# Performance work log

Hardware: AMD Instinct MI355X
Metric: run time of the kernel (lower is better)

The kernel has to match this reference:

```python
import jax, jax.numpy as jnp
import numpy as np

DIM = 1024
HEADS = 16
HEAD_DIM = DIM // HEADS
ROPE_BASE = 500000.0
SCALE = HEAD_DIM ** -0.5


def _rope_cos_sin(T, dtype=jnp.float32):
    inv_freq = 1.0 / (ROPE_BASE ** (jnp.arange(0, HEAD_DIM, 2, dtype=jnp.float32) / HEAD_DIM))
    t = jnp.arange(T, dtype=jnp.float32)
    freqs = t[:, None] * inv_freq[None, :]            # (T, hd/2)
    emb = jnp.concatenate([freqs, freqs], axis=-1)    # (T, hd)
    return jnp.cos(emb).astype(dtype), jnp.sin(emb).astype(dtype)


def _rotate_half(x):
    x1, x2 = jnp.split(x, 2, axis=-1)
    return jnp.concatenate([-x2, x1], axis=-1)


def _apply_rope(x, cos, sin):
    # x: (B,H,T,hd); cos/sin: (T,hd)
    return x * cos + _rotate_half(x) * sin


def setup_inputs() -> dict:
    key = jax.random.key(0)
    k1, k2, k3 = jax.random.split(key, 3)
    B, T = 4, 4096
    x = jax.random.normal(k1, (B, T, DIM), dtype=jnp.float32)
    W_qkv = jax.random.normal(k2, (DIM, 3 * DIM), dtype=jnp.float32) * (DIM ** -0.5)
    W_out = jax.random.normal(k3, (DIM, DIM), dtype=jnp.float32) * (DIM ** -0.5)
    return {"x": x, "W_qkv": W_qkv, "W_out": W_out}


def reference(x, W_qkv, W_out):
    B, T, D = x.shape
    H, hd = HEADS, HEAD_DIM
    qkv = (x @ W_qkv).reshape(B, T, 3, H, hd).transpose(2, 0, 3, 1, 4)  # (3,B,H,T,hd)
    q, k, v = qkv[0], qkv[1], qkv[2]
    cos, sin = _rope_cos_sin(T, q.dtype)
    q = _apply_rope(q, cos, sin)
    k = _apply_rope(k, cos, sin)
    # linear attention: elu+1 feature map
    q_feat = jax.nn.elu(q * SCALE) + 1.0
    k_feat = jax.nn.elu(k) + 1.0
    kv = jnp.einsum('bhtd,bhtv->bhdv', k_feat, v)      # (B,H,hd,hd)
    k_sum = k_feat.sum(axis=2)                          # (B,H,hd)
    denom = jnp.maximum(jnp.einsum('bhtd,bhd->bht', q_feat, k_sum), 1e-6)
    out = jnp.einsum('bhtd,bhdv->bhtv', q_feat, kv) / denom[..., None]
    out = out.transpose(0, 2, 1, 3).reshape(B, T, D)
    return out @ W_out
```

## Files before the change

### kernel.cpp

```cpp
#include <hip/hip_runtime.h>
#include <hip/hip_bf16.h>

typedef __bf16 bf16;
typedef bf16 bf16x4 __attribute__((ext_vector_type(4)));
typedef bf16 bf16x8 __attribute__((ext_vector_type(8)));
typedef float f32x4 __attribute__((ext_vector_type(4)));

#define GLD_LDS16(gptr, lptr) \
  __builtin_amdgcn_global_load_lds((const __attribute__((address_space(1))) unsigned int*)(gptr), \
                                   (__attribute__((address_space(3))) unsigned int*)(lptr), 16, 0, 0)

__global__ __launch_bounds__(256) void f32_to_bf16(const float* __restrict__ in,
                                                   bf16* __restrict__ out) {
  const size_t i = ((size_t)blockIdx.x * 256 + threadIdx.x) * 8;
  float4 a = *(const float4*)(in + i);
  float4 b = *(const float4*)(in + i + 4);
  bf16x8 o;
  o[0] = (bf16)a.x; o[1] = (bf16)a.y; o[2] = (bf16)a.z; o[3] = (bf16)a.w;
  o[4] = (bf16)b.x; o[5] = (bf16)b.y; o[6] = (bf16)b.z; o[7] = (bf16)b.w;
  *(bf16x8*)(out + i) = o;
}

__global__ __launch_bounds__(256) void transpose_f32_bf16(const float* __restrict__ in,
                                                          bf16* __restrict__ out,
                                                          int R, int C) {
  __shared__ float tile[32][33];
  const int bx = blockIdx.x * 32;
  const int by = blockIdx.y * 32;
  const int tx = threadIdx.x & 31;
  const int ty = threadIdx.x >> 5;
#pragma unroll
  for (int i = 0; i < 4; i++) {
    int r = by + ty + i * 8;
    tile[ty + i * 8][tx] = in[(size_t)r * C + bx + tx];
  }
  __syncthreads();
#pragma unroll
  for (int i = 0; i < 4; i++) {
    int r = bx + ty + i * 8;
    out[(size_t)r * R + by + tx] = (bf16)tile[tx][ty + i * 8];
  }
}

__global__ __launch_bounds__(256) void rope_tab(float2* __restrict__ ctab) {
  const int idx = blockIdx.x * 256 + threadIdx.x;
  const int t = idx >> 5, f = idx & 31;
  const float invf = (float)exp(-((double)f / 32.0) * log(500000.0));
  float sn, cs;
  sincosf((float)t * invf, &sn, &cs);
  ctab[idx] = make_float2(cs, sn);
}

__device__ __forceinline__ void gemm256_core(const bf16* __restrict__ A,
                                             const bf16* __restrict__ BT,
                                             const int K, const int m0, const int n0,
                                             bf16* __restrict__ As, bf16* __restrict__ Bs,
                                             f32x4 acc[8][4]) {
  const int tid = threadIdx.x;
  const int lane = tid & 63;
  const int w = tid >> 6;
  const int wm = w >> 2, wn = w & 3;

#pragma unroll
  for (int i = 0; i < 8; i++)
#pragma unroll
    for (int j = 0; j < 4; j++) acc[i][j] = f32x4{0.f, 0.f, 0.f, 0.f};

  const int lch = (tid & 3) ^ ((tid >> 3) & 3);
  const bf16* Ag = A + (size_t)(m0 + (tid >> 2)) * K + lch * 8;
  const bf16* Bg = BT + (size_t)(n0 + (tid >> 2)) * K + lch * 8;
  const int wb = w * 512;

#define STG(kh, db, k0)                                                   \
  do {                                                                    \
    bf16* aD = As + ((db) * 2 + (kh)) * 8192 + wb;                        \
    bf16* bD = Bs + ((db) * 2 + (kh)) * 8192 + wb;                        \
    const size_t go = (size_t)(k0) + (kh) * 32;                           \
    GLD_LDS16(Ag + go, aD);                                               \
    GLD_LDS16(Ag + (size_t)128 * K + go, aD + 4096);                      \
    GLD_LDS16(Bg + go, bD);                                               \
    GLD_LDS16(Bg + (size_t)128 * K + go, bD + 4096);                      \
  } while (0)

  const int fr = lane & 15;
  const int kq = lane >> 4;
  const int frow = fr * 32 + ((kq ^ ((fr >> 1) & 3)) << 3);
  const int aro = wm * 4096;
  const int bro = wn * 2048;

#define LOADFRAGS(kh, db)                                                 \
  const bf16* Ap = As + ((db) * 2 + (kh)) * 8192 + aro + frow;            \
  const bf16* Bp = Bs + ((db) * 2 + (kh)) * 8192 + bro + frow;            \
  bf16x8 af[8], bv[4];                                                    \
  _Pragma("unroll") for (int mi = 0; mi < 8; mi++)                        \
      af[mi] = *(const bf16x8*)(Ap + mi * 512);                           \
  _Pragma("unroll") for (int ni = 0; ni < 4; ni++)                        \
      bv[ni] = *(const bf16x8*)(Bp + ni * 512);

#define MFMA32                                                            \
  __builtin_amdgcn_s_setprio(1);                                          \
  _Pragma("unroll") for (int mi = 0; mi < 8; mi++)                        \
  _Pragma("unroll") for (int ni = 0; ni < 4; ni++)                        \
      acc[mi][ni] = __builtin_amdgcn_mfma_f32_16x16x32_bf16(              \
          af[mi], bv[ni], acc[mi][ni], 0, 0, 0);                          \
  __builtin_amdgcn_s_setprio(0);

  STG(0, 0, 0);
  STG(1, 0, 0);
  if (K > 64) {
    STG(0, 1, 64);
    asm volatile("s_waitcnt vmcnt(8)" ::: "memory");
  } else {
    asm volatile("s_waitcnt vmcnt(4)" ::: "memory");
  }
  __builtin_amdgcn_s_barrier();

  const int NT = K >> 6;
  for (int kt = 0; kt < NT; ++kt) {
    const int db = kt & 1;
    {
      LOADFRAGS(0, db);
      if (kt + 1 < NT) STG(1, db ^ 1, (kt + 1) * 64);
      __builtin_amdgcn_s_barrier();
      asm volatile("s_waitcnt lgkmcnt(0)" ::: "memory");
      __builtin_amdgcn_sched_barrier(0);
      MFMA32;
      if (kt + 1 < NT) asm volatile("s_waitcnt vmcnt(8)" ::: "memory");
      else             asm volatile("s_waitcnt vmcnt(0)" ::: "memory");
      __builtin_amdgcn_s_barrier();
    }
    {
      LOADFRAGS(1, db);
      if (kt + 2 < NT) STG(0, db, (kt + 2) * 64);
      __builtin_amdgcn_s_barrier();
      asm volatile("s_waitcnt lgkmcnt(0)" ::: "memory");
      __builtin_amdgcn_sched_barrier(0);
      MFMA32;
      if (kt + 2 < NT)      asm volatile("s_waitcnt vmcnt(8)" ::: "memory");
      else if (kt + 1 < NT) asm volatile("s_waitcnt vmcnt(4)" ::: "memory");
      __builtin_amdgcn_s_barrier();
    }
  }
#undef STG
#undef LOADFRAGS
#undef MFMA32
}

__device__ __forceinline__ void xcd_tile(int& m0, int& n0) {
  const int gx = gridDim.x;
  const int nwg = gx * gridDim.y;
  const int orig = blockIdx.y * gx + blockIdx.x;
  const int cpx = nwg >> 3;
  const int swb = (orig & 7) * cpx + (orig >> 3);
  m0 = (swb / gx) * 256;
  n0 = (swb % gx) * 256;
}

__global__ __launch_bounds__(512, 2) void gemm_qkv_fused(const bf16* __restrict__ A,
                                                         const bf16* __restrict__ BT,
                                                         const float2* __restrict__ ctab,
                                                         bf16* __restrict__ qfB,
                                                         bf16* __restrict__ kfB,
                                                         bf16* __restrict__ vfB) {
  __shared__ __attribute__((aligned(16))) bf16 As[32768];
  __shared__ __attribute__((aligned(16))) bf16 Bs[32768];
  const int K = 1024;
  int m0, n0;
  xcd_tile(m0, n0);

  f32x4 acc[8][4];
  gemm256_core(A, BT, K, m0, n0, As, Bs, acc);

  const int lane = threadIdx.x & 63;
  const int w = threadIdx.x >> 6;
  const int wm = w >> 2, wn = w & 3;
  const int fr15 = lane & 15;
  const int cb = n0 + wn * 64;
  const int p = cb >> 10;
  const int hh = (cb & 1023) >> 6;
  const int row00 = m0 + wm * 128 + ((lane >> 4) << 2);
  const int b = row00 >> 12;
  const size_t base0 = ((size_t)(b * 16 + hh)) * 4096 * 64;

  if (p == 2) {
#pragma unroll
    for (int mi = 0; mi < 8; mi++)
#pragma unroll
      for (int r = 0; r < 4; r++) {
        const int tloc = (row00 + mi * 16 + r) & 4095;
        bf16* dst = vfB + base0 + (size_t)tloc * 64;
#pragma unroll
        for (int ni = 0; ni < 4; ni++) dst[fr15 + ni * 16] = (bf16)acc[mi][ni][r];
      }
  } else {
    bf16* outp = (p == 0) ? qfB : kfB;
    const float scl = (p == 0) ? 0.125f : 1.0f;
#pragma unroll
    for (int mi = 0; mi < 8; mi++)
#pragma unroll
      for (int r = 0; r < 4; r++) {
        const int tloc = (row00 + mi * 16 + r) & 4095;
        const float2* ct = ctab + tloc * 32;
        bf16* dst = outp + base0 + (size_t)tloc * 64;
#pragma unroll
        for (int ni = 0; ni < 2; ni++) {
          const float2 cs2 = ct[fr15 + ni * 16];
          const float x1 = acc[mi][ni][r], x2 = acc[mi][ni + 2][r];
          const float r1 = (x1 * cs2.x - x2 * cs2.y) * scl;
          const float r2 = (x2 * cs2.x + x1 * cs2.y) * scl;
          dst[fr15 + ni * 16] = (bf16)(r1 > 0.f ? r1 + 1.f : __expf(r1));
          dst[fr15 + ni * 16 + 32] = (bf16)(r2 > 0.f ? r2 + 1.f : __expf(r2));
        }
      }
  }
}

__global__ __launch_bounds__(512, 2) void gemm_bt_f32(const bf16* __restrict__ A,
                                                      const bf16* __restrict__ BT,
                                                      float* __restrict__ C,
                                                      int N, int K) {
  __shared__ __attribute__((aligned(16))) bf16 As[32768];
  __shared__ __attribute__((aligned(16))) bf16 Bs[32768];
  int m0, n0;
  xcd_tile(m0, n0);

  f32x4 acc[8][4];
  gemm256_core(A, BT, K, m0, n0, As, Bs, acc);

  const int lane = threadIdx.x & 63;
  const int w = threadIdx.x >> 6;
  const int wm = w >> 2, wn = w & 3;
  const int col0 = n0 + wn * 64 + (lane & 15);
  const int row00 = m0 + wm * 128 + ((lane >> 4) << 2);
#pragma unroll
  for (int mi = 0; mi < 8; mi++)
#pragma unroll
    for (int ni = 0; ni < 4; ni++)
#pragma unroll
      for (int r = 0; r < 4; r++)
        C[(size_t)(row00 + mi * 16 + r) * N + col0 + ni * 16] = acc[mi][ni][r];
}

__global__ __launch_bounds__(256) void attn_kv(const bf16* __restrict__ kfB,
                                               const bf16* __restrict__ vfB,
                                               float* __restrict__ kvg,
                                               float* __restrict__ ksumg) {
  const int bh = blockIdx.x;
  const int t0 = blockIdx.y * 256;
  __shared__ __attribute__((aligned(16))) float kfs[32][68];
  __shared__ __attribute__((aligned(16))) float vfs[32][68];
  const int tid = threadIdx.x;
  const int dq = tid & 15, g = tid >> 4;
  const int tl = tid >> 3, ch = (tid & 7) * 8;

  f32x4 acc[4];
#pragma unroll
  for (int r = 0; r < 4; r++) acc[r] = f32x4{0.f, 0.f, 0.f, 0.f};
  float ksa[4] = {0.f, 0.f, 0.f, 0.f};

  for (int sc = 0; sc < 8; sc++) {
    const size_t rowb = ((size_t)bh * 4096 + t0 + sc * 32 + tl) * 64 + ch;
    bf16x8 k8 = *(const bf16x8*)(kfB + rowb);
    bf16x8 v8 = *(const bf16x8*)(vfB + rowb);
    f32x4 ka, kb, va, vb;
#pragma unroll
    for (int j = 0; j < 4; j++) {
      ka[j] = (float)k8[j]; kb[j] = (float)k8[j + 4];
      va[j] = (float)v8[j]; vb[j] = (float)v8[j + 4];
    }
    *(f32x4*)&kfs[tl][ch] = ka;
    *(f32x4*)&kfs[tl][ch + 4] = kb;
    *(f32x4*)&vfs[tl][ch] = va;
    *(f32x4*)&vfs[tl][ch + 4] = vb;
    __syncthreads();

#pragma unroll 8
    for (int t = 0; t < 32; t++) {
      f32x4 kq = *(const f32x4*)&kfs[t][dq * 4];
      f32x4 vq = *(const f32x4*)&vfs[t][g * 4];
#pragma unroll
      for (int r = 0; r < 4; r++) {
#pragma unroll
        for (int c = 0; c < 4; c++) acc[r][c] += kq[r] * vq[c];
      }
      if (g == 0) {
#pragma unroll
        for (int r = 0; r < 4; r++) ksa[r] += kq[r];
      }
    }
    __syncthreads();
  }

#pragma unroll
  for (int r = 0; r < 4; r++)
#pragma unroll
    for (int c = 0; c < 4; c++)
      atomicAdd(&kvg[(size_t)bh * 4096 + (dq * 4 + r) * 64 + g * 4 + c], acc[r][c]);
  if (g == 0) {
#pragma unroll
    for (int r = 0; r < 4; r++) atomicAdd(&ksumg[bh * 64 + dq * 4 + r], ksa[r]);
  }
}

__global__ __launch_bounds__(256) void attn_out(const bf16* __restrict__ qfB,
                                                const float* __restrict__ kvg,
                                                const float* __restrict__ ksumg,
                                                bf16* __restrict__ attn) {
  const int bh = blockIdx.y;
  const int b = bh >> 4, h = bh & 15;
  const int t0 = blockIdx.x * 64;
  __shared__ __attribute__((aligned(16))) float qf[64][68];
  __shared__ __attribute__((aligned(16))) float kvs[64][64];
  __shared__ __attribute__((aligned(16))) float ksums[64];
  const int tid = threadIdx.x;

#pragma unroll
  for (int j = 0; j < 2; j++) {
    int chunk = tid + 256 * j;
    int tl = chunk >> 3, col = (chunk & 7) * 8;
    bf16x8 r = *(const bf16x8*)(qfB + ((size_t)bh * 4096 + t0 + tl) * 64 + col);
    f32x4 a, bb;
#pragma unroll
    for (int q = 0; q < 4; q++) { a[q] = (float)r[q]; bb[q] = (float)r[q + 4]; }
    *(f32x4*)&qf[tl][col] = a;
    *(f32x4*)&qf[tl][col + 4] = bb;
  }
#pragma unroll
  for (int j = 0; j < 4; j++) {
    int idx = tid + 256 * j;
    *(float4*)&kvs[idx >> 4][(idx & 15) * 4] = *(const float4*)&kvg[(size_t)bh * 4096 + idx * 4];
  }
  if (tid < 64) ksums[tid] = ksumg[bh * 64 + tid];
  __syncthreads();

  const int tr = tid >> 4, cc = tid & 15;
  f32x4 acc[4];
#pragma unroll
  for (int r = 0; r < 4; r++) acc[r] = f32x4{0.f, 0.f, 0.f, 0.f};
  f32x4 dn = f32x4{0.f, 0.f, 0.f, 0.f};

  for (int d2 = 0; d2 < 64; d2++) {
    f32x4 kv4 = *(const f32x4*)&kvs[d2][cc * 4];
    float ks = ksums[d2];
#pragma unroll
    for (int r = 0; r < 4; r++) {
      float qv = qf[tr * 4 + r][d2];
      acc[r] += qv * kv4;
      dn[r] += qv * ks;
    }
  }

#pragma unroll
  for (int r = 0; r < 4; r++) {
    const float rdn = 1.f / fmaxf(dn[r], 1e-6f);
    bf16x4 o;
#pragma unroll
    for (int c = 0; c < 4; c++) o[c] = (bf16)(acc[r][c] * rdn);
    *(bf16x4*)(attn + ((size_t)(b * 4096) + t0 + tr * 4 + r) * 1024 + h * 64 + cc * 4) = o;
  }
}

extern "C" void kernel_launch(void* const* d_in, const int* in_sizes, int n_in,
                              void* d_out, int out_size, void* d_ws, size_t ws_size,
                              hipStream_t stream) {
  if (ws_size < 177225728ULL) return;

  const float* x = (const float*)d_in[0];
  const float* Wqkv = (const float*)d_in[1];
  const float* Wout = (const float*)d_in[2];
  float* out = (float*)d_out;
  char* ws = (char*)d_ws;

  float* kvg = (float*)(ws);
  float* ksumg = (float*)(ws + 1048576);
  bf16* WqkvT = (bf16*)(ws + 1064960);
  bf16* WoutT = (bf16*)(ws + 7356416);
  bf16* attn = (bf16*)(ws + 9453568);
  float2* ctab = (float2*)(ws + 9453568);
  bf16* qfB = (bf16*)(ws + 43008000);
  bf16* kfB = (bf16*)(ws + 76562432);
  bf16* vfB = (bf16*)(ws + 110116864);
  bf16* xB = (bf16*)(ws + 143671296);

  hipMemsetAsync(ws, 0, 1048576 + 16384, stream);

  rope_tab<<<512, 256, 0, stream>>>(ctab);
  f32_to_bf16<<<16777216 / (256 * 8), 256, 0, stream>>>(x, xB);
  transpose_f32_bf16<<<dim3(3072 / 32, 1024 / 32), 256, 0, stream>>>(Wqkv, WqkvT, 1024, 3072);
  transpose_f32_bf16<<<dim3(1024 / 32, 1024 / 32), 256, 0, stream>>>(Wout, WoutT, 1024, 1024);

  gemm_qkv_fused<<<dim3(3072 / 256, 16384 / 256), 512, 0, stream>>>(xB, WqkvT, ctab, qfB, kfB, vfB);

  attn_kv<<<dim3(64, 16), 256, 0, stream>>>(kfB, vfB, kvg, ksumg);
  attn_out<<<dim3(64, 64), 256, 0, stream>>>(qfB, kvg, ksumg, attn);

  gemm_bt_f32<<<dim3(1024 / 256, 16384 / 256), 512, 0, stream>>>(attn, WoutT, out, 1024, 1024);
}
```

Before: 385.3 us.

## Store K/V feature-major and compute KV outer product with MFMA

The QKV GEMM epilogue now writes K features and V in a feature-major (transposed) layout, so the KV reduction can load contiguous time slices straight into MFMA 16x16x32 bf16 operands. This replaces the scalar fp32 LDS outer product. Partial KV tiles from the four waves are summed in LDS before the global atomics, and the key sum is computed with cross-lane shuffles. The small prep kernels (rope table and both weight transposes) are merged into one launch, and attn_out handles 256 tokens per block so the kv tile is loaded once per block instead of once per 64 tokens. The cost is strided transposed stores in the GEMM epilogue, more LDS in the KV kernel, and fewer blocks for attn_out.

Result: slower. 438.7 us (+13.8%).

```diff
diff --git a/kernel.cpp b/kernel.cpp
--- a/kernel.cpp
+++ b/kernel.cpp
@@ -21,34 +21,43 @@
   *(bf16x8*)(out + i) = o;
 }
 
-__global__ __launch_bounds__(256) void transpose_f32_bf16(const float* __restrict__ in,
-                                                          bf16* __restrict__ out,
-                                                          int R, int C) {
+__global__ __launch_bounds__(256) void prep(const float* __restrict__ Wqkv,
+                                            const float* __restrict__ Wout,
+                                            bf16* __restrict__ WqkvT,
+                                            bf16* __restrict__ WoutT,
+                                            float2* __restrict__ ctab) {
+  const int bid = blockIdx.x;
+  if (bid < 512) {
+    const int idx = bid * 256 + threadIdx.x;
+    const int t = idx >> 5, f = idx & 31;
+    const float invf = (float)exp(-((double)f / 32.0) * log(500000.0));
+    float sn, cs;
+    sincosf((float)t * invf, &sn, &cs);
+    ctab[idx] = make_float2(cs, sn);
+    return;
+  }
   __shared__ float tile[32][33];
-  const int bx = blockIdx.x * 32;
-  const int by = blockIdx.y * 32;
+  const float* in;
+  bf16* out;
+  int R, C, bx, by;
+  if (bid < 3584) {
+    const int t = bid - 512;
+    in = Wqkv; out = WqkvT; R = 1024; C = 3072;
+    bx = (t % 96) * 32; by = (t / 96) * 32;
+  } else {
+    const int t = bid - 3584;
+    in = Wout; out = WoutT; R = 1024; C = 1024;
+    bx = (t & 31) * 32; by = (t >> 5) * 32;
+  }
   const int tx = threadIdx.x & 31;
   const int ty = threadIdx.x >> 5;
 #pragma unroll
-  for (int i = 0; i < 4; i++) {
-    int r = by + ty + i * 8;
-    tile[ty + i * 8][tx] = in[(size_t)r * C + bx + tx];
-  }
+  for (int i = 0; i < 4; i++)
+    tile[ty + i * 8][tx] = in[(size_t)(by + ty + i * 8) * C + bx + tx];
   __syncthreads();
 #pragma unroll
-  for (int i = 0; i < 4; i++) {
-    int r = bx + ty + i * 8;
-    out[(size_t)r * R + by + tx] = (bf16)tile[tx][ty + i * 8];
-  }
-}
-
-__global__ __launch_bounds__(256) void rope_tab(float2* __restrict__ ctab) {
-  const int idx = blockIdx.x * 256 + threadIdx.x;
-  const int t = idx >> 5, f = idx & 31;
-  const float invf = (float)exp(-((double)f / 32.0) * log(500000.0));
-  float sn, cs;
-  sincosf((float)t * invf, &sn, &cs);
-  ctab[idx] = make_float2(cs, sn);
+  for (int i = 0; i < 4; i++)
+    out[(size_t)(bx + ty + i * 8) * R + by + tx] = (bf16)tile[tx][ty + i * 8];
 }
 
 __device__ __forceinline__ void gemm256_core(const bf16* __restrict__ A,
@@ -160,8 +169,8 @@
                                                          const bf16* __restrict__ BT,
                                                          const float2* __restrict__ ctab,
                                                          bf16* __restrict__ qfB,
-                                                         bf16* __restrict__ kfB,
-                                                         bf16* __restrict__ vfB) {
+                                                         bf16* __restrict__ kfT,
+                                                         bf16* __restrict__ vfT) {
   __shared__ __attribute__((aligned(16))) bf16 As[32768];
   __shared__ __attribute__((aligned(16))) bf16 Bs[32768];
   const int K = 1024;
@@ -181,33 +190,52 @@
   const int row00 = m0 + wm * 128 + ((lane >> 4) << 2);
   const int b = row00 >> 12;
   const size_t base0 = ((size_t)(b * 16 + hh)) * 4096 * 64;
+  const int tb = row00 & 4095;
 
   if (p == 2) {
 #pragma unroll
     for (int mi = 0; mi < 8; mi++)
 #pragma unroll
-      for (int r = 0; r < 4; r++) {
-        const int tloc = (row00 + mi * 16 + r) & 4095;
-        bf16* dst = vfB + base0 + (size_t)tloc * 64;
-#pragma unroll
-        for (int ni = 0; ni < 4; ni++) dst[fr15 + ni * 16] = (bf16)acc[mi][ni][r];
+      for (int ni = 0; ni < 4; ni++) {
+        bf16x4 o;
+#pragma unroll
+        for (int r = 0; r < 4; r++) o[r] = (bf16)acc[mi][ni][r];
+        *(bf16x4*)(vfT + base0 + (size_t)(fr15 + ni * 16) * 4096 + tb + mi * 16) = o;
+      }
+  } else if (p == 1) {
+#pragma unroll
+    for (int mi = 0; mi < 8; mi++)
+#pragma unroll
+      for (int ni = 0; ni < 2; ni++) {
+        bf16x4 olo, ohi;
+#pragma unroll
+        for (int r = 0; r < 4; r++) {
+          const int tloc = tb + mi * 16 + r;
+          const float2 cs2 = ctab[tloc * 32 + fr15 + ni * 16];
+          const float x1 = acc[mi][ni][r], x2 = acc[mi][ni + 2][r];
+          const float r1 = x1 * cs2.x - x2 * cs2.y;
+          const float r2 = x2 * cs2.x + x1 * cs2.y;
+          olo[r] = (bf16)(r1 > 0.f ? r1 + 1.f : __expf(r1));
+          ohi[r] = (bf16)(r2 > 0.f ? r2 + 1.f : __expf(r2));
+        }
+        bf16* dp = kfT + base0 + (size_t)(fr15 + ni * 16) * 4096 + tb + mi * 16;
+        *(bf16x4*)dp = olo;
+        *(bf16x4*)(dp + (size_t)32 * 4096) = ohi;
       }
   } else {
-    bf16* outp = (p == 0) ? qfB : kfB;
-    const float scl = (p == 0) ? 0.125f : 1.0f;
 #pragma unroll
     for (int mi = 0; mi < 8; mi++)
 #pragma unroll
       for (int r = 0; r < 4; r++) {
-        const int tloc = (row00 + mi * 16 + r) & 4095;
+        const int tloc = tb + mi * 16 + r;
         const float2* ct = ctab + tloc * 32;
-        bf16* dst = outp + base0 + (size_t)tloc * 64;
+        bf16* dst = qfB + base0 + (size_t)tloc * 64;
 #pragma unroll
         for (int ni = 0; ni < 2; ni++) {
           const float2 cs2 = ct[fr15 + ni * 16];
           const float x1 = acc[mi][ni][r], x2 = acc[mi][ni + 2][r];
-          const float r1 = (x1 * cs2.x - x2 * cs2.y) * scl;
-          const float r2 = (x2 * cs2.x + x1 * cs2.y) * scl;
+          const float r1 = (x1 * cs2.x - x2 * cs2.y) * 0.125f;
+          const float r2 = (x2 * cs2.x + x1 * cs2.y) * 0.125f;
           dst[fr15 + ni * 16] = (bf16)(r1 > 0.f ? r1 + 1.f : __expf(r1));
           dst[fr15 + ni * 16 + 32] = (bf16)(r2 > 0.f ? r2 + 1.f : __expf(r2));
         }
@@ -241,64 +269,77 @@
         C[(size_t)(row00 + mi * 16 + r) * N + col0 + ni * 16] = acc[mi][ni][r];
 }
 
-__global__ __launch_bounds__(256) void attn_kv(const bf16* __restrict__ kfB,
-                                               const bf16* __restrict__ vfB,
-                                               float* __restrict__ kvg,
-                                               float* __restrict__ ksumg) {
+__global__ __launch_bounds__(256) void attn_kv_mfma(const bf16* __restrict__ kfT,
+                                                    const bf16* __restrict__ vfT,
+                                                    float* __restrict__ kvg,
+                                                    float* __restrict__ ksumg) {
   const int bh = blockIdx.x;
-  const int t0 = blockIdx.y * 256;
-  __shared__ __attribute__((aligned(16))) float kfs[32][68];
-  __shared__ __attribute__((aligned(16))) float vfs[32][68];
+  const int kc = blockIdx.y;
   const int tid = threadIdx.x;
-  const int dq = tid & 15, g = tid >> 4;
-  const int tl = tid >> 3, ch = (tid & 7) * 8;
-
-  f32x4 acc[4];
-#pragma unroll
-  for (int r = 0; r < 4; r++) acc[r] = f32x4{0.f, 0.f, 0.f, 0.f};
-  float ksa[4] = {0.f, 0.f, 0.f, 0.f};
-
-  for (int sc = 0; sc < 8; sc++) {
-    const size_t rowb = ((size_t)bh * 4096 + t0 + sc * 32 + tl) * 64 + ch;
-    bf16x8 k8 = *(const bf16x8*)(kfB + rowb);
-    bf16x8 v8 = *(const bf16x8*)(vfB + rowb);
-    f32x4 ka, kb, va, vb;
-#pragma unroll
-    for (int j = 0; j < 4; j++) {
-      ka[j] = (float)k8[j]; kb[j] = (float)k8[j + 4];
-      va[j] = (float)v8[j]; vb[j] = (float)v8[j + 4];
-    }
-    *(f32x4*)&kfs[tl][ch] = ka;
-    *(f32x4*)&kfs[tl][ch + 4] = kb;
-    *(f32x4*)&vfs[tl][ch] = va;
-    *(f32x4*)&vfs[tl][ch + 4] = vb;
-    __syncthreads();
-
-#pragma unroll 8
-    for (int t = 0; t < 32; t++) {
-      f32x4 kq = *(const f32x4*)&kfs[t][dq * 4];
-      f32x4 vq = *(const f32x4*)&vfs[t][g * 4];
-#pragma unroll
-      for (int r = 0; r < 4; r++) {
-#pragma unroll
-        for (int c = 0; c < 4; c++) acc[r][c] += kq[r] * vq[c];
-      }
-      if (g == 0) {
-#pragma unroll
-        for (int r = 0; r < 4; r++) ksa[r] += kq[r];
-      }
-    }
-    __syncthreads();
-  }
-
-#pragma unroll
-  for (int r = 0; r < 4; r++)
-#pragma unroll
-    for (int c = 0; c < 4; c++)
-      atomicAdd(&kvg[(size_t)bh * 4096 + (dq * 4 + r) * 64 + g * 4 + c], acc[r][c]);
-  if (g == 0) {
-#pragma unroll
-    for (int r = 0; r < 4; r++) atomicAdd(&ksumg[bh * 64 + dq * 4 + r], ksa[r]);
+  const int lane = tid & 63;
+  const int w = tid >> 6;
+  const int fr = lane & 15;
+  const int kq = lane >> 4;
+
+  __shared__ __attribute__((aligned(16))) float kvp[4][64][68];
+
+  const size_t hb = (size_t)bh * 64 * 4096;
+  const int kbase = kc * 512 + w * 128 + kq * 8;
+
+  f32x4 acc[4][4];
+#pragma unroll
+  for (int i = 0; i < 4; i++)
+#pragma unroll
+    for (int j = 0; j < 4; j++) acc[i][j] = f32x4{0.f, 0.f, 0.f, 0.f};
+  float ks[4] = {0.f, 0.f, 0.f, 0.f};
+
+#pragma unroll
+  for (int c = 0; c < 4; c++) {
+    const int k0 = kbase + c * 32;
+    bf16x8 af[4], bv[4];
+#pragma unroll
+    for (int mi = 0; mi < 4; mi++)
+      af[mi] = *(const bf16x8*)(kfT + hb + (size_t)(mi * 16 + fr) * 4096 + k0);
+#pragma unroll
+    for (int ni = 0; ni < 4; ni++)
+      bv[ni] = *(const bf16x8*)(vfT + hb + (size_t)(ni * 16 + fr) * 4096 + k0);
+#pragma unroll
+    for (int mi = 0; mi < 4; mi++) {
+#pragma unroll
+      for (int ni = 0; ni < 4; ni++)
+        acc[mi][ni] = __builtin_amdgcn_mfma_f32_16x16x32_bf16(af[mi], bv[ni], acc[mi][ni], 0, 0, 0);
+#pragma unroll
+      for (int e = 0; e < 8; e++) ks[mi] += (float)af[mi][e];
+    }
+  }
+
+#pragma unroll
+  for (int mi = 0; mi < 4; mi++) {
+    ks[mi] += __shfl_xor(ks[mi], 16, 64);
+    ks[mi] += __shfl_xor(ks[mi], 32, 64);
+  }
+  if (kq == 0) {
+#pragma unroll
+    for (int mi = 0; mi < 4; mi++)
+      atomicAdd(&ksumg[bh * 64 + mi * 16 + fr], ks[mi]);
+  }
+
+#pragma unroll
+  for (int mi = 0; mi < 4; mi++)
+#pragma unroll
+    for (int ni = 0; ni < 4; ni++)
+#pragma unroll
+      for (int r = 0; r < 4; r++)
+        kvp[w][mi * 16 + kq * 4 + r][ni * 16 + fr] = acc[mi][ni][r];
+  __syncthreads();
+
+  const int d = tid >> 2;
+  const int v0 = (tid & 3) * 16;
+#pragma unroll
+  for (int j = 0; j < 16; j++) {
+    const float s = kvp[0][d][v0 + j] + kvp[1][d][v0 + j] +
+                    kvp[2][d][v0 + j] + kvp[3][d][v0 + j];
+    atomicAdd(&kvg[(size_t)bh * 4096 + d * 64 + v0 + j], s);
   }
 }
 
@@ -308,55 +349,61 @@
                                                 bf16* __restrict__ attn) {
   const int bh = blockIdx.y;
   const int b = bh >> 4, h = bh & 15;
-  const int t0 = blockIdx.x * 64;
+  const int t0 = blockIdx.x * 256;
   __shared__ __attribute__((aligned(16))) float qf[64][68];
   __shared__ __attribute__((aligned(16))) float kvs[64][64];
   __shared__ __attribute__((aligned(16))) float ksums[64];
   const int tid = threadIdx.x;
 
 #pragma unroll
-  for (int j = 0; j < 2; j++) {
-    int chunk = tid + 256 * j;
-    int tl = chunk >> 3, col = (chunk & 7) * 8;
-    bf16x8 r = *(const bf16x8*)(qfB + ((size_t)bh * 4096 + t0 + tl) * 64 + col);
-    f32x4 a, bb;
-#pragma unroll
-    for (int q = 0; q < 4; q++) { a[q] = (float)r[q]; bb[q] = (float)r[q + 4]; }
-    *(f32x4*)&qf[tl][col] = a;
-    *(f32x4*)&qf[tl][col + 4] = bb;
-  }
-#pragma unroll
   for (int j = 0; j < 4; j++) {
     int idx = tid + 256 * j;
     *(float4*)&kvs[idx >> 4][(idx & 15) * 4] = *(const float4*)&kvg[(size_t)bh * 4096 + idx * 4];
   }
   if (tid < 64) ksums[tid] = ksumg[bh * 64 + tid];
-  __syncthreads();
 
   const int tr = tid >> 4, cc = tid & 15;
-  f32x4 acc[4];
-#pragma unroll
-  for (int r = 0; r < 4; r++) acc[r] = f32x4{0.f, 0.f, 0.f, 0.f};
-  f32x4 dn = f32x4{0.f, 0.f, 0.f, 0.f};
-
-  for (int d2 = 0; d2 < 64; d2++) {
-    f32x4 kv4 = *(const f32x4*)&kvs[d2][cc * 4];
-    float ks = ksums[d2];
+
+  for (int sub = 0; sub < 4; sub++) {
+    if (sub) __syncthreads();
+    const int ts = t0 + sub * 64;
+#pragma unroll
+    for (int j = 0; j < 2; j++) {
+      int chunk = tid + 256 * j;
+      int tl = chunk >> 3, col = (chunk & 7) * 8;
+      bf16x8 r = *(const bf16x8*)(qfB + ((size_t)bh * 4096 + ts + tl) * 64 + col);
+      f32x4 a, bb;
+#pragma unroll
+      for (int q = 0; q < 4; q++) { a[q] = (float)r[q]; bb[q] = (float)r[q + 4]; }
+      *(f32x4*)&qf[tl][col] = a;
+      *(f32x4*)&qf[tl][col + 4] = bb;
+    }
+    __syncthreads();
+
+    f32x4 acc[4];
+#pragma unroll
+    for (int r = 0; r < 4; r++) acc[r] = f32x4{0.f, 0.f, 0.f, 0.f};
+    f32x4 dn = f32x4{0.f, 0.f, 0.f, 0.f};
+
+    for (int d2 = 0; d2 < 64; d2++) {
+      f32x4 kv4 = *(const f32x4*)&kvs[d2][cc * 4];
+      float kss = ksums[d2];
+#pragma unroll
+      for (int r = 0; r < 4; r++) {
+        float qv = qf[tr * 4 + r][d2];
+        acc[r] += qv * kv4;
+        dn[r] += qv * kss;
+      }
+    }
+
 #pragma unroll
     for (int r = 0; r < 4; r++) {
-      float qv = qf[tr * 4 + r][d2];
-      acc[r] += qv * kv4;
-      dn[r] += qv * ks;
-    }
-  }
-
-#pragma unroll
-  for (int r = 0; r < 4; r++) {
-    const float rdn = 1.f / fmaxf(dn[r], 1e-6f);
-    bf16x4 o;
-#pragma unroll
-    for (int c = 0; c < 4; c++) o[c] = (bf16)(acc[r][c] * rdn);
-    *(bf16x4*)(attn + ((size_t)(b * 4096) + t0 + tr * 4 + r) * 1024 + h * 64 + cc * 4) = o;
+      const float rdn = 1.f / fmaxf(dn[r], 1e-6f);
+      bf16x4 o;
+#pragma unroll
+      for (int c = 0; c < 4; c++) o[c] = (bf16)(acc[r][c] * rdn);
+      *(bf16x4*)(attn + ((size_t)(b * 4096) + ts + tr * 4 + r) * 1024 + h * 64 + cc * 4) = o;
+    }
   }
 }
 
@@ -378,21 +425,19 @@
   bf16* attn = (bf16*)(ws + 9453568);
   float2* ctab = (float2*)(ws + 9453568);
   bf16* qfB = (bf16*)(ws + 43008000);
-  bf16* kfB = (bf16*)(ws + 76562432);
-  bf16* vfB = (bf16*)(ws + 110116864);
+  bf16* kfT = (bf16*)(ws + 76562432);
+  bf16* vfT = (bf16*)(ws + 110116864);
   bf16* xB = (bf16*)(ws + 143671296);
 
   hipMemsetAsync(ws, 0, 1048576 + 16384, stream);
 
-  rope_tab<<<512, 256, 0, stream>>>(ctab);
+  prep<<<4608, 256, 0, stream>>>(Wqkv, Wout, WqkvT, WoutT, ctab);
   f32_to_bf16<<<16777216 / (256 * 8), 256, 0, stream>>>(x, xB);
-  transpose_f32_bf16<<<dim3(3072 / 32, 1024 / 32), 256, 0, stream>>>(Wqkv, WqkvT, 1024, 3072);
-  transpose_f32_bf16<<<dim3(1024 / 32, 1024 / 32), 256, 0, stream>>>(Wout, WoutT, 1024, 1024);
-
-  gemm_qkv_fused<<<dim3(3072 / 256, 16384 / 256), 512, 0, stream>>>(xB, WqkvT, ctab, qfB, kfB, vfB);
-
-  attn_kv<<<dim3(64, 16), 256, 0, stream>>>(kfB, vfB, kvg, ksumg);
-  attn_out<<<dim3(64, 64), 256, 0, stream>>>(qfB, kvg, ksumg, attn);
+
+  gemm_qkv_fused<<<dim3(3072 / 256, 16384 / 256), 512, 0, stream>>>(xB, WqkvT, ctab, qfB, kfT, vfT);
+
+  attn_kv_mfma<<<dim3(64, 8), 256, 0, stream>>>(kfT, vfT, kvg, ksumg);
+  attn_out<<<dim3(16, 64), 256, 0, stream>>>(qfB, kvg, ksumg, attn);
 
   gemm_bt_f32<<<dim3(1024 / 256, 16384 / 256), 512, 0, stream>>>(attn, WoutT, out, 1024, 1024);
 }
```
